# Optimization experiments

Hardware: AMD Instinct MI355X
Metric: run time of the kernel (lower is better)

## Reference

```python
import jax, jax.numpy as jnp
import numpy as np

WS = 7            # window size
N = WS * WS       # tokens per window (49)
DIM = 128
HEADS = 4
HEAD_DIM = DIM // HEADS
SCALE = HEAD_DIM ** -0.5
NW = 64           # number of windows (mask leading dim)
B_WIN = 4096      # B * nW


def _relative_position_index():
    coords = np.stack(np.meshgrid(np.arange(WS), np.arange(WS), indexing='ij'))  # (2,WS,WS)
    cf = coords.reshape(2, -1)                       # (2, N)
    rel = cf[:, :, None] - cf[:, None, :]            # (2, N, N)
    rel = rel.transpose(1, 2, 0).copy()              # (N, N, 2)
    rel[..., 0] += WS - 1
    rel[..., 1] += WS - 1
    rel[..., 0] *= 2 * WS - 1
    return rel.sum(-1)                               # (N, N) int

REL_IDX = jnp.asarray(_relative_position_index())


def setup_inputs() -> dict:
    key = jax.random.key(0)
    ks = jax.random.split(key, 7)
    return {
        'x': jax.random.normal(ks[0], (B_WIN, N, DIM), dtype=jnp.float32),
        'mask': jax.random.normal(ks[1], (NW, N, N), dtype=jnp.float32),
        'qkv_w': jax.random.normal(ks[2], (3 * DIM, DIM), dtype=jnp.float32) * 0.02,
        'qkv_b': jax.random.normal(ks[3], (3 * DIM,), dtype=jnp.float32) * 0.02,
        'proj_w': jax.random.normal(ks[4], (DIM, DIM), dtype=jnp.float32) * 0.02,
        'proj_b': jax.random.normal(ks[5], (DIM,), dtype=jnp.float32) * 0.02,
        'bias_table': jax.random.normal(ks[6], ((2 * WS - 1) ** 2, HEADS), dtype=jnp.float32) * 0.02,
    }


def reference(x, mask, qkv_w, qkv_b, proj_w, proj_b, bias_table):
    B_, n, C = x.shape
    # qkv projection: (B_, N, 3C) -> (3, B_, H, N, hd)
    qkv = (x @ qkv_w.T + qkv_b).reshape(B_, n, 3, HEADS, HEAD_DIM)
    qkv = jnp.transpose(qkv, (2, 0, 3, 1, 4))
    q, k, v = qkv[0], qkv[1], qkv[2]
    # scaled scores: (B_, H, N, N)
    attn = jnp.einsum('bhnd,bhmd->bhnm', q * SCALE, k)
    # gathered relative position bias: (N, N, H) -> (H, N, N)
    rel_bias = jnp.transpose(bias_table[REL_IDX], (2, 0, 1))
    attn = attn + rel_bias[None]
    # shifted-window mask: broadcast over batch groups and heads
    nW = mask.shape[0]
    attn = attn.reshape(B_ // nW, nW, HEADS, n, n) + mask[None, :, None]
    attn = attn.reshape(B_, HEADS, n, n)
    attn = jax.nn.softmax(attn, axis=-1)
    out = jnp.einsum('bhnm,bhmd->bhnd', attn, v)
    out = jnp.transpose(out, (0, 2, 1, 3)).reshape(B_, n, C)
    return out @ proj_w.T + proj_b
```

## Files before the change

### kernel.cpp

```cpp
#include <hip/hip_runtime.h>

#define QK_SCALE 0.17677669529663687f

typedef __attribute__((ext_vector_type(8))) short bf16x8;
typedef __attribute__((ext_vector_type(4))) short bf16x4;
typedef __attribute__((ext_vector_type(2))) short bf16x2;
typedef __attribute__((ext_vector_type(4))) float floatx4;

__device__ __forceinline__ unsigned short f2bf(float f) {
    unsigned int u = __float_as_uint(f);
    u += 0x7fffu + ((u >> 16) & 1u);
    return (unsigned short)(u >> 16);
}

__device__ __forceinline__ bf16x8 ld8_2x4(const short* p) {
    union { bf16x8 v8; bf16x4 v4[2]; } u;
    u.v4[0] = *(const bf16x4*)p;
    u.v4[1] = *(const bf16x4*)(p + 4);
    return u.v8;
}

__device__ __forceinline__ bf16x8 ld8_4x2(const short* p) {
    union { bf16x8 v8; bf16x2 v2[4]; } u;
    u.v2[0] = *(const bf16x2*)p;
    u.v2[1] = *(const bf16x2*)(p + 2);
    u.v2[2] = *(const bf16x2*)(p + 4);
    u.v2[3] = *(const bf16x2*)(p + 6);
    return u.v8;
}

__global__ __launch_bounds__(256) void prep_kernel(
    const float* __restrict__ qkv_w, const float* __restrict__ proj_w,
    const float* __restrict__ bias_table, const float* __restrict__ mask,
    unsigned short* __restrict__ wbf, float* __restrict__ cm2)
{
    int g = blockIdx.x * 256 + threadIdx.x;
    if (g < 49152) {
        wbf[g] = f2bf(qkv_w[g]);
    } else if (g < 65536) {
        wbf[g] = f2bf(proj_w[g - 49152]);
    } else if (g < 868352) {
        int t = g - 65536;
        int nt  = t & 3;
        int lid = (t >> 2) & 15;
        int t2  = t >> 6;
        int row = t2 % 49;
        int wh  = t2 / 49;
        int h   = wh & 3;
        int w   = wh >> 2;
        int col = nt * 16 + lid;
        float v;
        if (col < 49) {
            int idx = (row / 7 - col / 7 + 6) * 13 + (row % 7 - col % 7 + 6);
            v = mask[w * 2401 + row * 49 + col] + bias_table[idx * 4 + h];
        } else {
            v = -1e30f;
        }
        cm2[t] = v;
    }
}

__global__ __launch_bounds__(256, 3) void winattn_mfma(
    const float* __restrict__ x,
    const float* __restrict__ qkv_b,
    const float* __restrict__ proj_b,
    const unsigned short* __restrict__ wbf,
    const float* __restrict__ cm2,
    float* __restrict__ out)
{
    __shared__ __align__(16) short smem[26112];

    const int tid  = threadIdx.x;
    const int lane = tid & 63;
    const int lid  = lane & 15;
    const int quad = lane >> 4;
    const int h    = tid >> 6;
    const int b    = blockIdx.x;
    const int w    = b & 63;
    const int hq   = h * 6528;

    {
        const float4* xg = (const float4*)(x + (size_t)b * 6272);
        for (int i = tid; i < 1568; i += 256) {
            int n = i >> 5, c4 = i & 31;
            float4 v = xg[i];
            ushort4 u;
            u.x = f2bf(v.x); u.y = f2bf(v.y); u.z = f2bf(v.z); u.w = f2bf(v.w);
            *(ushort4*)&smem[n * 136 + c4 * 4] = u;
        }
        ushort4 z; z.x = 0; z.y = 0; z.z = 0; z.w = 0;
        for (int i = tid; i < 510; i += 256)
            *(ushort4*)&smem[49 * 136 + i * 4] = z;
    }
    __syncthreads();

    bf16x8 ax[4][4];
    #pragma unroll
    for (int mt = 0; mt < 4; ++mt)
        #pragma unroll
        for (int kb = 0; kb < 4; ++kb)
            ax[mt][kb] = *(const bf16x8*)&smem[(mt * 16 + lid) * 136 + kb * 32 + quad * 8];
    __syncthreads();

    const floatx4 z4 = {0.f, 0.f, 0.f, 0.f};

    #pragma unroll
    for (int t = 0; t < 6; ++t) {
        const int cb = (t < 2) ? (h * 32 + t * 16)
                     : (t < 4) ? (128 + h * 32 + (t - 2) * 16)
                               : (256 + h * 32 + (t - 4) * 16);
        const unsigned short* wr = wbf + (size_t)(cb + lid) * 128 + quad * 8;
        floatx4 acc[4] = {z4, z4, z4, z4};
        #pragma unroll
        for (int kb = 0; kb < 4; ++kb) {
            bf16x8 bw = *(const bf16x8*)(wr + kb * 32);
            #pragma unroll
            for (int mt = 0; mt < 4; ++mt)
                acc[mt] = __builtin_amdgcn_mfma_f32_16x16x32_bf16(ax[mt][kb], bw, acc[mt], 0, 0, 0);
        }
        const float bias = qkv_b[cb + lid];
        #pragma unroll
        for (int mt = 0; mt < 4; ++mt) {
            #pragma unroll
            for (int r = 0; r < 4; ++r) {
                const int row = mt * 16 + quad * 4 + r;
                const float v = acc[mt][r] + bias;
                if (t < 2) {
                    smem[hq + row * 34 + t * 16 + lid] = (short)f2bf(v * QK_SCALE);
                } else if (t < 4) {
                    smem[hq + 2176 + row * 34 + (t - 2) * 16 + lid] = (short)f2bf(v);
                } else {
                    smem[hq + 4352 + ((t - 4) * 16 + lid) * 68 + row] = (short)f2bf(v);
                }
            }
        }
    }

    const float4* cm2b = (const float4*)cm2 + ((size_t)(w * 4 + h) * 49) * 16 + lid;
    float4 cmv[4][4];
    #pragma unroll
    for (int r = 0; r < 4; ++r)
        cmv[0][r] = cm2b[(quad * 4 + r) * 16];

    bf16x8 aq[4], bk[4];
    #pragma unroll
    for (int mt = 0; mt < 4; ++mt)
        aq[mt] = ld8_4x2(&smem[hq + (mt * 16 + lid) * 34 + quad * 8]);
    #pragma unroll
    for (int nt = 0; nt < 4; ++nt)
        bk[nt] = ld8_4x2(&smem[hq + 2176 + (nt * 16 + lid) * 34 + quad * 8]);

    floatx4 sacc[4][4];
    #pragma unroll
    for (int mt = 0; mt < 4; ++mt)
        #pragma unroll
        for (int nt = 0; nt < 4; ++nt)
            sacc[mt][nt] = __builtin_amdgcn_mfma_f32_16x16x32_bf16(aq[mt], bk[nt], z4, 0, 0, 0);

    float invs[4][4];
    #pragma unroll
    for (int mt = 0; mt < 4; ++mt) {
        if (mt < 3) {
            #pragma unroll
            for (int r = 0; r < 4; ++r) {
                const int row  = (mt + 1) * 16 + quad * 4 + r;
                const int rowc = (row < 49) ? row : 48;
                cmv[mt + 1][r] = cm2b[rowc * 16];
            }
        }
        #pragma unroll
        for (int r = 0; r < 4; ++r) {
            const int row = mt * 16 + quad * 4 + r;
            float sv[4];
            #pragma unroll
            for (int nt = 0; nt < 4; ++nt)
                sv[nt] = sacc[mt][nt][r] + cmv[mt][r][nt];
            float mx = fmaxf(fmaxf(sv[0], sv[1]), fmaxf(sv[2], sv[3]));
            #pragma unroll
            for (int d = 1; d < 16; d <<= 1) mx = fmaxf(mx, __shfl_xor(mx, d));
            float sum = 0.f;
            #pragma unroll
            for (int nt = 0; nt < 4; ++nt) { float p = __expf(sv[nt] - mx); sv[nt] = p; sum += p; }
            #pragma unroll
            for (int d = 1; d < 16; d <<= 1) sum += __shfl_xor(sum, d);
            invs[mt][r] = 1.f / sum;
            #pragma unroll
            for (int nt = 0; nt < 4; ++nt)
                smem[hq + row * 68 + nt * 16 + lid] = (short)f2bf(sv[nt]);
        }
    }

    bf16x8 bv[2][2];
    #pragma unroll
    for (int nt2 = 0; nt2 < 2; ++nt2)
        #pragma unroll
        for (int kb2 = 0; kb2 < 2; ++kb2)
            bv[nt2][kb2] = ld8_2x4(&smem[hq + 4352 + (nt2 * 16 + lid) * 68 + kb2 * 32 + quad * 8]);

    floatx4 oacc[4][2] = {{z4, z4}, {z4, z4}, {z4, z4}, {z4, z4}};
    #pragma unroll
    for (int mt = 0; mt < 4; ++mt) {
        #pragma unroll
        for (int kb2 = 0; kb2 < 2; ++kb2) {
            bf16x8 ap = ld8_2x4(&smem[hq + (mt * 16 + lid) * 68 + kb2 * 32 + quad * 8]);
            #pragma unroll
            for (int nt2 = 0; nt2 < 2; ++nt2)
                oacc[mt][nt2] = __builtin_amdgcn_mfma_f32_16x16x32_bf16(ap, bv[nt2][kb2], oacc[mt][nt2], 0, 0, 0);
        }
    }

    __syncthreads();

    #pragma unroll
    for (int mt = 0; mt < 4; ++mt)
        #pragma unroll
        for (int nt2 = 0; nt2 < 2; ++nt2)
            #pragma unroll
            for (int r = 0; r < 4; ++r) {
                const int row = mt * 16 + quad * 4 + r;
                smem[row * 136 + h * 32 + nt2 * 16 + lid] =
                    (short)f2bf(oacc[mt][nt2][r] * invs[mt][r]);
            }
    __syncthreads();

    bf16x8 aa[4][4];
    #pragma unroll
    for (int mt = 0; mt < 4; ++mt)
        #pragma unroll
        for (int kb = 0; kb < 4; ++kb)
            aa[mt][kb] = *(const bf16x8*)&smem[(mt * 16 + lid) * 136 + kb * 32 + quad * 8];

    float* outb = out + (size_t)b * 6272;
    #pragma unroll
    for (int nt = 0; nt < 2; ++nt) {
        const int cb = h * 32 + nt * 16;
        const unsigned short* wr = wbf + 49152 + (size_t)(cb + lid) * 128 + quad * 8;
        floatx4 acc[4] = {z4, z4, z4, z4};
        #pragma unroll
        for (int kb = 0; kb < 4; ++kb) {
            bf16x8 bw = *(const bf16x8*)(wr + kb * 32);
            #pragma unroll
            for (int mt = 0; mt < 4; ++mt)
                acc[mt] = __builtin_amdgcn_mfma_f32_16x16x32_bf16(aa[mt][kb], bw, acc[mt], 0, 0, 0);
        }
        const float pb = proj_b[cb + lid];
        #pragma unroll
        for (int mt = 0; mt < 4; ++mt)
            #pragma unroll
            for (int r = 0; r < 4; ++r) {
                const int row = mt * 16 + quad * 4 + r;
                if (row < 49)
                    outb[row * 128 + cb + lid] = acc[mt][r] + pb;
            }
    }
}

extern "C" void kernel_launch(void* const* d_in, const int* in_sizes, int n_in,
                              void* d_out, int out_size, void* d_ws, size_t ws_size,
                              hipStream_t stream) {
    (void)in_sizes; (void)n_in; (void)out_size; (void)ws_size;
    const float* x          = (const float*)d_in[0];
    const float* mask       = (const float*)d_in[1];
    const float* qkv_w      = (const float*)d_in[2];
    const float* qkv_b      = (const float*)d_in[3];
    const float* proj_w     = (const float*)d_in[4];
    const float* proj_b     = (const float*)d_in[5];
    const float* bias_table = (const float*)d_in[6];

    unsigned short* wbf = (unsigned short*)d_ws;
    float* cm2          = (float*)((char*)d_ws + 131072);

    prep_kernel<<<3392, 256, 0, stream>>>(qkv_w, proj_w, bias_table, mask, wbf, cm2);
    winattn_mfma<<<4096, 256, 0, stream>>>(x, qkv_b, proj_b, wbf, cm2, (float*)d_out);
}
```

Before: 276.5 us.

## Split each head across two waves with 512-thread blocks

Doubles the block to 8 waves so that two waves share each head. In the QKV projection each wave computes one 16-column half of q, k and v. In attention and the output projection each wave handles half of the row tiles. This cuts per-wave register use and serial MFMA work to raise parallelism and latency hiding. It adds two more block-wide barriers, and the new __launch_bounds__(512, 6) requests a much tighter register budget, which may cause spills.

Measured after the change: 476.7 us. +72.4%, slower.

```diff
diff --git a/kernel.cpp b/kernel.cpp
--- a/kernel.cpp
+++ b/kernel.cpp
@@ -60,7 +60,7 @@
     }
 }
 
-__global__ __launch_bounds__(256, 3) void winattn_mfma(
+__global__ __launch_bounds__(512, 6) void winattn_mfma(
     const float* __restrict__ x,
     const float* __restrict__ qkv_b,
     const float* __restrict__ proj_b,
@@ -74,14 +74,16 @@
     const int lane = tid & 63;
     const int lid  = lane & 15;
     const int quad = lane >> 4;
-    const int h    = tid >> 6;
+    const int wid  = tid >> 6;
+    const int h    = wid >> 1;
+    const int half = wid & 1;
     const int b    = blockIdx.x;
     const int w    = b & 63;
     const int hq   = h * 6528;
 
     {
         const float4* xg = (const float4*)(x + (size_t)b * 6272);
-        for (int i = tid; i < 1568; i += 256) {
+        for (int i = tid; i < 1568; i += 512) {
             int n = i >> 5, c4 = i & 31;
             float4 v = xg[i];
             ushort4 u;
@@ -89,7 +91,7 @@
             *(ushort4*)&smem[n * 136 + c4 * 4] = u;
         }
         ushort4 z; z.x = 0; z.y = 0; z.z = 0; z.w = 0;
-        for (int i = tid; i < 510; i += 256)
+        for (int i = tid; i < 510; i += 512)
             *(ushort4*)&smem[49 * 136 + i * 4] = z;
     }
     __syncthreads();
@@ -105,10 +107,8 @@
     const floatx4 z4 = {0.f, 0.f, 0.f, 0.f};
 
     #pragma unroll
-    for (int t = 0; t < 6; ++t) {
-        const int cb = (t < 2) ? (h * 32 + t * 16)
-                     : (t < 4) ? (128 + h * 32 + (t - 2) * 16)
-                               : (256 + h * 32 + (t - 4) * 16);
+    for (int j = 0; j < 3; ++j) {
+        const int cb = j * 128 + h * 32 + half * 16;
         const unsigned short* wr = wbf + (size_t)(cb + lid) * 128 + quad * 8;
         floatx4 acc[4] = {z4, z4, z4, z4};
         #pragma unroll
@@ -125,56 +125,62 @@
             for (int r = 0; r < 4; ++r) {
                 const int row = mt * 16 + quad * 4 + r;
                 const float v = acc[mt][r] + bias;
-                if (t < 2) {
-                    smem[hq + row * 34 + t * 16 + lid] = (short)f2bf(v * QK_SCALE);
-                } else if (t < 4) {
-                    smem[hq + 2176 + row * 34 + (t - 2) * 16 + lid] = (short)f2bf(v);
+                if (j == 0) {
+                    smem[hq + row * 34 + half * 16 + lid] = (short)f2bf(v * QK_SCALE);
+                } else if (j == 1) {
+                    smem[hq + 2176 + row * 34 + half * 16 + lid] = (short)f2bf(v);
                 } else {
-                    smem[hq + 4352 + ((t - 4) * 16 + lid) * 68 + row] = (short)f2bf(v);
+                    smem[hq + 4352 + (half * 16 + lid) * 68 + row] = (short)f2bf(v);
                 }
             }
         }
     }
+    __syncthreads();
 
     const float4* cm2b = (const float4*)cm2 + ((size_t)(w * 4 + h) * 49) * 16 + lid;
-    float4 cmv[4][4];
-    #pragma unroll
-    for (int r = 0; r < 4; ++r)
-        cmv[0][r] = cm2b[(quad * 4 + r) * 16];
-
-    bf16x8 aq[4], bk[4];
-    #pragma unroll
-    for (int mt = 0; mt < 4; ++mt)
-        aq[mt] = ld8_4x2(&smem[hq + (mt * 16 + lid) * 34 + quad * 8]);
+    float4 cmv[2][4];
+    #pragma unroll
+    for (int r = 0; r < 4; ++r) {
+        const int row  = (2 * half) * 16 + quad * 4 + r;
+        const int rowc = (row < 49) ? row : 48;
+        cmv[0][r] = cm2b[rowc * 16];
+    }
+
+    bf16x8 aq[2], bk[4];
+    #pragma unroll
+    for (int m = 0; m < 2; ++m)
+        aq[m] = ld8_4x2(&smem[hq + ((2 * half + m) * 16 + lid) * 34 + quad * 8]);
     #pragma unroll
     for (int nt = 0; nt < 4; ++nt)
         bk[nt] = ld8_4x2(&smem[hq + 2176 + (nt * 16 + lid) * 34 + quad * 8]);
 
-    floatx4 sacc[4][4];
-    #pragma unroll
-    for (int mt = 0; mt < 4; ++mt)
+    floatx4 sacc[2][4];
+    #pragma unroll
+    for (int m = 0; m < 2; ++m)
         #pragma unroll
         for (int nt = 0; nt < 4; ++nt)
-            sacc[mt][nt] = __builtin_amdgcn_mfma_f32_16x16x32_bf16(aq[mt], bk[nt], z4, 0, 0, 0);
-
-    float invs[4][4];
-    #pragma unroll
-    for (int mt = 0; mt < 4; ++mt) {
-        if (mt < 3) {
-            #pragma unroll
-            for (int r = 0; r < 4; ++r) {
-                const int row  = (mt + 1) * 16 + quad * 4 + r;
+            sacc[m][nt] = __builtin_amdgcn_mfma_f32_16x16x32_bf16(aq[m], bk[nt], z4, 0, 0, 0);
+
+    __syncthreads();
+
+    float invs[2][4];
+    #pragma unroll
+    for (int m = 0; m < 2; ++m) {
+        if (m < 1) {
+            #pragma unroll
+            for (int r = 0; r < 4; ++r) {
+                const int row  = (2 * half + 1) * 16 + quad * 4 + r;
                 const int rowc = (row < 49) ? row : 48;
-                cmv[mt + 1][r] = cm2b[rowc * 16];
+                cmv[1][r] = cm2b[rowc * 16];
             }
         }
         #pragma unroll
         for (int r = 0; r < 4; ++r) {
-            const int row = mt * 16 + quad * 4 + r;
+            const int row = (2 * half + m) * 16 + quad * 4 + r;
             float sv[4];
             #pragma unroll
             for (int nt = 0; nt < 4; ++nt)
-                sv[nt] = sacc[mt][nt][r] + cmv[mt][r][nt];
+                sv[nt] = sacc[m][nt][r] + cmv[m][r][nt];
             float mx = fmaxf(fmaxf(sv[0], sv[1]), fmaxf(sv[2], sv[3]));
             #pragma unroll
             for (int d = 1; d < 16; d <<= 1) mx = fmaxf(mx, __shfl_xor(mx, d));
@@ -183,7 +189,7 @@
             for (int nt = 0; nt < 4; ++nt) { float p = __expf(sv[nt] - mx); sv[nt] = p; sum += p; }
             #pragma unroll
             for (int d = 1; d < 16; d <<= 1) sum += __shfl_xor(sum, d);
-            invs[mt][r] = 1.f / sum;
+            invs[m][r] = 1.f / sum;
             #pragma unroll
             for (int nt = 0; nt < 4; ++nt)
                 smem[hq + row * 68 + nt * 16 + lid] = (short)f2bf(sv[nt]);
@@ -197,60 +203,60 @@
         for (int kb2 = 0; kb2 < 2; ++kb2)
             bv[nt2][kb2] = ld8_2x4(&smem[hq + 4352 + (nt2 * 16 + lid) * 68 + kb2 * 32 + quad * 8]);
 
-    floatx4 oacc[4][2] = {{z4, z4}, {z4, z4}, {z4, z4}, {z4, z4}};
-    #pragma unroll
-    for (int mt = 0; mt < 4; ++mt) {
+    floatx4 oacc[2][2] = {{z4, z4}, {z4, z4}};
+    #pragma unroll
+    for (int m = 0; m < 2; ++m) {
         #pragma unroll
         for (int kb2 = 0; kb2 < 2; ++kb2) {
-            bf16x8 ap = ld8_2x4(&smem[hq + (mt * 16 + lid) * 68 + kb2 * 32 + quad * 8]);
+            bf16x8 ap = ld8_2x4(&smem[hq + ((2 * half + m) * 16 + lid) * 68 + kb2 * 32 + quad * 8]);
             #pragma unroll
             for (int nt2 = 0; nt2 < 2; ++nt2)
-                oacc[mt][nt2] = __builtin_amdgcn_mfma_f32_16x16x32_bf16(ap, bv[nt2][kb2], oacc[mt][nt2], 0, 0, 0);
-        }
-    }
-
-    __syncthreads();
-
-    #pragma unroll
-    for (int mt = 0; mt < 4; ++mt)
+                oacc[m][nt2] = __builtin_amdgcn_mfma_f32_16x16x32_bf16(ap, bv[nt2][kb2], oacc[m][nt2], 0, 0, 0);
+        }
+    }
+
+    __syncthreads();
+
+    #pragma unroll
+    for (int m = 0; m < 2; ++m)
         #pragma unroll
         for (int nt2 = 0; nt2 < 2; ++nt2)
             #pragma unroll
             for (int r = 0; r < 4; ++r) {
-                const int row = mt * 16 + quad * 4 + r;
+                const int row = (2 * half + m) * 16 + quad * 4 + r;
                 smem[row * 136 + h * 32 + nt2 * 16 + lid] =
-                    (short)f2bf(oacc[mt][nt2][r] * invs[mt][r]);
-            }
-    __syncthreads();
-
-    bf16x8 aa[4][4];
-    #pragma unroll
-    for (int mt = 0; mt < 4; ++mt)
+                    (short)f2bf(oacc[m][nt2][r] * invs[m][r]);
+            }
+    __syncthreads();
+
+    bf16x8 aa[2][4];
+    #pragma unroll
+    for (int m = 0; m < 2; ++m)
         #pragma unroll
         for (int kb = 0; kb < 4; ++kb)
-            aa[mt][kb] = *(const bf16x8*)&smem[(mt * 16 + lid) * 136 + kb * 32 + quad * 8];
+            aa[m][kb] = *(const bf16x8*)&smem[((2 * half + m) * 16 + lid) * 136 + kb * 32 + quad * 8];
 
     float* outb = out + (size_t)b * 6272;
     #pragma unroll
     for (int nt = 0; nt < 2; ++nt) {
         const int cb = h * 32 + nt * 16;
         const unsigned short* wr = wbf + 49152 + (size_t)(cb + lid) * 128 + quad * 8;
-        floatx4 acc[4] = {z4, z4, z4, z4};
+        floatx4 acc[2] = {z4, z4};
         #pragma unroll
         for (int kb = 0; kb < 4; ++kb) {
             bf16x8 bw = *(const bf16x8*)(wr + kb * 32);
             #pragma unroll
-            for (int mt = 0; mt < 4; ++mt)
-                acc[mt] = __builtin_amdgcn_mfma_f32_16x16x32_bf16(aa[mt][kb], bw, acc[mt], 0, 0, 0);
+            for (int m = 0; m < 2; ++m)
+                acc[m] = __builtin_amdgcn_mfma_f32_16x16x32_bf16(aa[m][kb], bw, acc[m], 0, 0, 0);
         }
         const float pb = proj_b[cb + lid];
         #pragma unroll
-        for (int mt = 0; mt < 4; ++mt)
-            #pragma unroll
-            for (int r = 0; r < 4; ++r) {
-                const int row = mt * 16 + quad * 4 + r;
+        for (int m = 0; m < 2; ++m)
+            #pragma unroll
+            for (int r = 0; r < 4; ++r) {
+                const int row = (2 * half + m) * 16 + quad * 4 + r;
                 if (row < 49)
-                    outb[row * 128 + cb + lid] = acc[mt][r] + pb;
+                    outb[row * 128 + cb + lid] = acc[m][r] + pb;
             }
     }
 }
@@ -271,5 +277,5 @@
     float* cm2          = (float*)((char*)d_ws + 131072);
 
     prep_kernel<<<3392, 256, 0, stream>>>(qkv_w, proj_w, bias_table, mask, wbf, cm2);
-    winattn_mfma<<<4096, 256, 0, stream>>>(x, qkv_b, proj_b, wbf, cm2, (float*)d_out);
-}
+    winattn_mfma<<<4096, 512, 0, stream>>>(x, qkv_b, proj_b, wbf, cm2, (float*)d_out);
+}
```

## Store bias+mask in MFMA accumulator layout and prefetch weight fragments

Applied to the files above, without the earlier changes.

The prep kernel now writes the combined relative-position bias and mask directly in the MFMA accumulator fragment layout, padded rows included. The main kernel loads it straight into the score accumulators and uses it as the MFMA C input, which removes the per-element add and the staggered loads from the softmax loop. QKV weight fragments are double-buffered one tile ahead, and projection weights are loaded before the barrier. This raises register pressure and makes the precomputed buffer larger (about 1.05M floats instead of 0.8M).

Measured after the change: 270.1 us. 1.02x faster.

```diff
diff --git a/kernel.cpp b/kernel.cpp
--- a/kernel.cpp
+++ b/kernel.cpp
@@ -32,31 +32,33 @@
 __global__ __launch_bounds__(256) void prep_kernel(
     const float* __restrict__ qkv_w, const float* __restrict__ proj_w,
     const float* __restrict__ bias_table, const float* __restrict__ mask,
-    unsigned short* __restrict__ wbf, float* __restrict__ cm2)
+    unsigned short* __restrict__ wbf, float* __restrict__ cm3)
 {
     int g = blockIdx.x * 256 + threadIdx.x;
     if (g < 49152) {
         wbf[g] = f2bf(qkv_w[g]);
     } else if (g < 65536) {
         wbf[g] = f2bf(proj_w[g - 49152]);
-    } else if (g < 868352) {
+    } else if (g < 1114112) {
         int t = g - 65536;
-        int nt  = t & 3;
-        int lid = (t >> 2) & 15;
-        int t2  = t >> 6;
-        int row = t2 % 49;
-        int wh  = t2 / 49;
-        int h   = wh & 3;
-        int w   = wh >> 2;
-        int col = nt * 16 + lid;
+        int r    = t & 3;
+        int lane = (t >> 2) & 63;
+        int nt   = (t >> 8) & 3;
+        int mt   = (t >> 10) & 3;
+        int wh   = t >> 12;
+        int h    = wh & 3;
+        int w    = wh >> 2;
+        int row  = mt * 16 + (lane >> 4) * 4 + r;
+        int col  = nt * 16 + (lane & 15);
+        int rowc = (row < 49) ? row : 48;
         float v;
         if (col < 49) {
-            int idx = (row / 7 - col / 7 + 6) * 13 + (row % 7 - col % 7 + 6);
-            v = mask[w * 2401 + row * 49 + col] + bias_table[idx * 4 + h];
+            int idx = (rowc / 7 - col / 7 + 6) * 13 + (rowc % 7 - col % 7 + 6);
+            v = mask[w * 2401 + rowc * 49 + col] + bias_table[idx * 4 + h];
         } else {
             v = -1e30f;
         }
-        cm2[t] = v;
+        cm3[t] = v;
     }
 }
 
@@ -65,7 +67,7 @@
     const float* __restrict__ qkv_b,
     const float* __restrict__ proj_b,
     const unsigned short* __restrict__ wbf,
-    const float* __restrict__ cm2,
+    const float* __restrict__ cm3,
     float* __restrict__ out)
 {
     __shared__ __align__(16) short smem[26112];
@@ -104,20 +106,32 @@
 
     const floatx4 z4 = {0.f, 0.f, 0.f, 0.f};
 
+    bf16x8 bwc[4], bwn[4];
+    {
+        const unsigned short* wr0 = wbf + (size_t)(h * 32 + lid) * 128 + quad * 8;
+        #pragma unroll
+        for (int kb = 0; kb < 4; ++kb)
+            bwc[kb] = *(const bf16x8*)(wr0 + kb * 32);
+    }
     #pragma unroll
     for (int t = 0; t < 6; ++t) {
-        const int cb = (t < 2) ? (h * 32 + t * 16)
-                     : (t < 4) ? (128 + h * 32 + (t - 2) * 16)
-                               : (256 + h * 32 + (t - 4) * 16);
-        const unsigned short* wr = wbf + (size_t)(cb + lid) * 128 + quad * 8;
+        const int part = t >> 1;
+        const int c    = t & 1;
+        const int cb   = part * 128 + h * 32 + c * 16;
+        if (t < 5) {
+            const int tn = t + 1;
+            const int cbn = (tn >> 1) * 128 + h * 32 + (tn & 1) * 16;
+            const unsigned short* wrn = wbf + (size_t)(cbn + lid) * 128 + quad * 8;
+            #pragma unroll
+            for (int kb = 0; kb < 4; ++kb)
+                bwn[kb] = *(const bf16x8*)(wrn + kb * 32);
+        }
         floatx4 acc[4] = {z4, z4, z4, z4};
         #pragma unroll
-        for (int kb = 0; kb < 4; ++kb) {
-            bf16x8 bw = *(const bf16x8*)(wr + kb * 32);
+        for (int kb = 0; kb < 4; ++kb)
             #pragma unroll
             for (int mt = 0; mt < 4; ++mt)
-                acc[mt] = __builtin_amdgcn_mfma_f32_16x16x32_bf16(ax[mt][kb], bw, acc[mt], 0, 0, 0);
-        }
+                acc[mt] = __builtin_amdgcn_mfma_f32_16x16x32_bf16(ax[mt][kb], bwc[kb], acc[mt], 0, 0, 0);
         const float bias = qkv_b[cb + lid];
         #pragma unroll
         for (int mt = 0; mt < 4; ++mt) {
@@ -125,22 +139,26 @@
             for (int r = 0; r < 4; ++r) {
                 const int row = mt * 16 + quad * 4 + r;
                 const float v = acc[mt][r] + bias;
-                if (t < 2) {
-                    smem[hq + row * 34 + t * 16 + lid] = (short)f2bf(v * QK_SCALE);
-                } else if (t < 4) {
-                    smem[hq + 2176 + row * 34 + (t - 2) * 16 + lid] = (short)f2bf(v);
+                if (part == 0) {
+                    smem[hq + row * 34 + c * 16 + lid] = (short)f2bf(v * QK_SCALE);
+                } else if (part == 1) {
+                    smem[hq + 2176 + row * 34 + c * 16 + lid] = (short)f2bf(v);
                 } else {
-                    smem[hq + 4352 + ((t - 4) * 16 + lid) * 68 + row] = (short)f2bf(v);
+                    smem[hq + 4352 + (c * 16 + lid) * 68 + row] = (short)f2bf(v);
                 }
             }
         }
-    }
-
-    const float4* cm2b = (const float4*)cm2 + ((size_t)(w * 4 + h) * 49) * 16 + lid;
-    float4 cmv[4][4];
-    #pragma unroll
-    for (int r = 0; r < 4; ++r)
-        cmv[0][r] = cm2b[(quad * 4 + r) * 16];
+        #pragma unroll
+        for (int kb = 0; kb < 4; ++kb) bwc[kb] = bwn[kb];
+    }
+
+    floatx4 sacc[4][4];
+    const floatx4* cm3b = (const floatx4*)cm3 + (size_t)((w * 4 + h) * 16) * 64 + lane;
+    #pragma unroll
+    for (int mt = 0; mt < 4; ++mt)
+        #pragma unroll
+        for (int nt = 0; nt < 4; ++nt)
+            sacc[mt][nt] = cm3b[(mt * 4 + nt) * 64];
 
     bf16x8 aq[4], bk[4];
     #pragma unroll
@@ -150,31 +168,22 @@
     for (int nt = 0; nt < 4; ++nt)
         bk[nt] = ld8_4x2(&smem[hq + 2176 + (nt * 16 + lid) * 34 + quad * 8]);
 
-    floatx4 sacc[4][4];
     #pragma unroll
     for (int mt = 0; mt < 4; ++mt)
         #pragma unroll
         for (int nt = 0; nt < 4; ++nt)
-            sacc[mt][nt] = __builtin_amdgcn_mfma_f32_16x16x32_bf16(aq[mt], bk[nt], z4, 0, 0, 0);
+            sacc[mt][nt] = __builtin_amdgcn_mfma_f32_16x16x32_bf16(aq[mt], bk[nt], sacc[mt][nt], 0, 0, 0);
 
     float invs[4][4];
     #pragma unroll
     for (int mt = 0; mt < 4; ++mt) {
-        if (mt < 3) {
-            #pragma unroll
-            for (int r = 0; r < 4; ++r) {
-                const int row  = (mt + 1) * 16 + quad * 4 + r;
-                const int rowc = (row < 49) ? row : 48;
-                cmv[mt + 1][r] = cm2b[rowc * 16];
-            }
-        }
         #pragma unroll
         for (int r = 0; r < 4; ++r) {
             const int row = mt * 16 + quad * 4 + r;
             float sv[4];
             #pragma unroll
             for (int nt = 0; nt < 4; ++nt)
-                sv[nt] = sacc[mt][nt][r] + cmv[mt][r][nt];
+                sv[nt] = sacc[mt][nt][r];
             float mx = fmaxf(fmaxf(sv[0], sv[1]), fmaxf(sv[2], sv[3]));
             #pragma unroll
             for (int d = 1; d < 16; d <<= 1) mx = fmaxf(mx, __shfl_xor(mx, d));
@@ -207,6 +216,15 @@
             for (int nt2 = 0; nt2 < 2; ++nt2)
                 oacc[mt][nt2] = __builtin_amdgcn_mfma_f32_16x16x32_bf16(ap, bv[nt2][kb2], oacc[mt][nt2], 0, 0, 0);
         }
+    }
+
+    bf16x8 pw[2][4];
+    #pragma unroll
+    for (int nt = 0; nt < 2; ++nt) {
+        const unsigned short* wr = wbf + 49152 + (size_t)(h * 32 + nt * 16 + lid) * 128 + quad * 8;
+        #pragma unroll
+        for (int kb = 0; kb < 4; ++kb)
+            pw[nt][kb] = *(const bf16x8*)(wr + kb * 32);
     }
 
     __syncthreads();
@@ -234,15 +252,12 @@
     #pragma unroll
     for (int nt = 0; nt < 2; ++nt) {
         const int cb = h * 32 + nt * 16;
-        const unsigned short* wr = wbf + 49152 + (size_t)(cb + lid) * 128 + quad * 8;
         floatx4 acc[4] = {z4, z4, z4, z4};
         #pragma unroll
-        for (int kb = 0; kb < 4; ++kb) {
-            bf16x8 bw = *(const bf16x8*)(wr + kb * 32);
+        for (int kb = 0; kb < 4; ++kb)
             #pragma unroll
             for (int mt = 0; mt < 4; ++mt)
-                acc[mt] = __builtin_amdgcn_mfma_f32_16x16x32_bf16(aa[mt][kb], bw, acc[mt], 0, 0, 0);
-        }
+                acc[mt] = __builtin_amdgcn_mfma_f32_16x16x32_bf16(aa[mt][kb], pw[nt][kb], acc[mt], 0, 0, 0);
         const float pb = proj_b[cb + lid];
         #pragma unroll
         for (int mt = 0; mt < 4; ++mt)
@@ -268,8 +283,8 @@
     const float* bias_table = (const float*)d_in[6];
 
     unsigned short* wbf = (unsigned short*)d_ws;
-    float* cm2          = (float*)((char*)d_ws + 131072);
-
-    prep_kernel<<<3392, 256, 0, stream>>>(qkv_w, proj_w, bias_table, mask, wbf, cm2);
-    winattn_mfma<<<4096, 256, 0, stream>>>(x, qkv_b, proj_b, wbf, cm2, (float*)d_out);
-}
+    float* cm3          = (float*)((char*)d_ws + 131072);
+
+    prep_kernel<<<4352, 256, 0, stream>>>(qkv_w, proj_w, bias_table, mask, wbf, cm3);
+    winattn_mfma<<<4096, 256, 0, stream>>>(x, qkv_b, proj_b, wbf, cm3, (float*)d_out);
+}
```
